# Performance work log

Hardware: AMD Instinct MI355X
Metric: run time of the kernel (lower is better)

The kernel has to match this reference:

```python
import jax, jax.numpy as jnp
import numpy as np

N = 2048
D_T = 256; D_F = 256
E_T = 32; E_F = 32; E_C = 128
C = 5; Q = 512


def setup_inputs() -> dict:
    key = jax.random.key(0)
    ks = jax.random.split(key, 12)
    # full graph minus self-loops, row-major (matches dense_to_sparse ordering)
    r, c = np.meshgrid(np.arange(N), np.arange(N), indexing='ij')
    m = r != c
    edge_index = jnp.asarray(np.stack([r[m], c[m]]), dtype=jnp.int32)  # [2, N*(N-1)]
    E = edge_index.shape[1]
    s = 0.02
    return {
        'time_features': jax.random.normal(ks[0], (N, D_T), jnp.float32),
        'edge_index': edge_index,
        'time_edge_weight': jax.random.uniform(ks[1], (E,), jnp.float32),
        'freq_features': jax.random.normal(ks[2], (N, D_F), jnp.float32),
        'freq_edge_weight': jax.random.uniform(ks[3], (E,), jnp.float32),
        'labels': jax.random.randint(ks[4], (N,), 0, C, jnp.int32),
        'num_classes': C,
        'query_size': Q,
        'Wt': jax.random.normal(ks[5], (D_T, E_T), jnp.float32) * s,
        'bt': jnp.zeros((E_T,), jnp.float32),
        'Wf': jax.random.normal(ks[6], (D_F, E_F), jnp.float32) * s,
        'bf': jnp.zeros((E_F,), jnp.float32),
        'Wc': jax.random.normal(ks[7], (E_T + E_F + C, E_C), jnp.float32) * s,
        'bc': jnp.zeros((E_C,), jnp.float32),
        'Wo': jax.random.normal(ks[8], (E_C, C), jnp.float32) * s,
        'bo': jnp.zeros((C,), jnp.float32),
    }


def _gcn(x, A, W, b):
    # torch_geometric GCNConv: D^{-1/2}(A + I)D^{-1/2} (X W) + b
    n = A.shape[0]
    Ah = A + jnp.eye(n, dtype=A.dtype)
    deg = Ah.sum(axis=1)
    dis = jnp.where(deg > 0, jax.lax.rsqrt(deg), 0.0)
    return (dis[:, None] * Ah * dis[None, :]) @ (x @ W) + b


def reference(time_features, edge_index, time_edge_weight, freq_features,
              freq_edge_weight, labels, num_classes, query_size,
              Wt, bt, Wf, bf, Wc, bc, Wo, bo):
    n = time_features.shape[0]
    lrelu = lambda z: jax.nn.leaky_relu(z, 0.01)

    def dense_adj(w):  # A[dst, src] = w
        return jnp.zeros((n, n), w.dtype).at[edge_index[1], edge_index[0]].add(w)

    te = lrelu(_gcn(time_features, dense_adj(time_edge_weight), Wt, bt))
    fe = lrelu(_gcn(freq_features, dense_adj(freq_edge_weight), Wf, bf))

    # to_one_hot: one_hot[:n - query_size, labels] = 1 -> support rows get 1 in
    # every column that appears anywhere in `labels`
    cols = jnp.zeros((num_classes,), te.dtype).at[labels].set(1.0)
    rowmask = (jnp.arange(n) < (n - query_size)).astype(te.dtype)
    one_hot = rowmask[:, None] * cols[None, :]

    feats = jnp.concatenate([te, fe, one_hot], axis=-1)  # [n, E_T+E_F+C]

    # graph_construction (no_grad in original): 1 / (L1 distance over the
    # non-one-hot dims + 1e-5), zero diagonal
    fd = jax.lax.stop_gradient(feats[:, : feats.shape[1] - num_classes])
    dist = jnp.sum(jnp.abs(fd[:, None, :] - fd[None, :, :]), axis=-1)  # [n, n]
    Aw = (1.0 / (dist + 1e-5)) * (1.0 - jnp.eye(n, dtype=feats.dtype))

    emb = lrelu(_gcn(feats, Aw, Wc, bc))
    return emb @ Wo + bo
```

## Files before the change

### kernel.cpp

```cpp
#include <hip/hip_runtime.h>
#include <hip/hip_bf16.h>

#define N 2048
#define NM1 2047
#define DT 256
#define ET 32
#define EC 128
#define NC 5
#define FS 80
#define FD 69
#define KC_ET 16
#define KC_EC 16

typedef __hip_bfloat16 bf16;

__global__ __launch_bounds__(256) void k_deg_label(const float* __restrict__ tw,
                                                   const float* __restrict__ fw,
                                                   const int* __restrict__ labels,
                                                   float* __restrict__ degT,
                                                   float* __restrict__ degF,
                                                   float* __restrict__ cols){
    int b = blockIdx.x;
    int t = threadIdx.x;
    if (b == 512){
        __shared__ float lc[NC];
        if (t < NC) lc[t] = 0.f;
        __syncthreads();
        for (int i = t; i < N; i += 256){
            int l = labels[i];
            if (l >= 0 && l < NC) lc[l] = 1.f;
        }
        __syncthreads();
        if (t < NC) cols[t] = lc[t];
        return;
    }
    int p = (b & 7)*256 + t;
    if (p >= NM1) return;
    int s0 = (b >> 3)*32;
    float lowT=0.f, highT=0.f, lowF=0.f, highF=0.f;
    #pragma unroll 8
    for (int r = 0; r < 32; ++r){
        int s = s0 + r;
        float vt = tw[(size_t)s*NM1 + p];
        float vf = fw[(size_t)s*NM1 + p];
        if (s <= p){ highT += vt; highF += vf; }
        else       { lowT  += vt; lowF  += vf; }
    }
    atomicAdd(&degT[p],   lowT);
    atomicAdd(&degF[p],   lowF);
    atomicAdd(&degT[p+1], highT);
    atomicAdd(&degF[p+1], highF);
}

__global__ __launch_bounds__(256) void k_xw2(const float* __restrict__ Xt,
                                             const float* __restrict__ Wt,
                                             const float* __restrict__ degT,
                                             float* __restrict__ Zt,
                                             const float* __restrict__ Xf,
                                             const float* __restrict__ Wf,
                                             const float* __restrict__ degF,
                                             float* __restrict__ Zf){
    const float* X   = blockIdx.y ? Xf   : Xt;
    const float* W   = blockIdx.y ? Wf   : Wt;
    const float* deg = blockIdx.y ? degF : degT;
    float*       Z   = blockIdx.y ? Zf   : Zt;
    __shared__ float Ws[DT*ET];
    __shared__ float Xs[8*DT];
    int t = threadIdx.x;
    for (int idx = t; idx < DT*ET; idx += 256) Ws[idx] = W[idx];
    int i0 = blockIdx.x*8;
    for (int idx = t; idx < 8*DT; idx += 256) Xs[idx] = X[(size_t)i0*DT + idx];
    __syncthreads();
    int r = t >> 5, f = t & 31;
    const float* xr = Xs + r*DT;
    float acc = 0.f;
    #pragma unroll 8
    for (int d = 0; d < DT; ++d) acc += xr[d]*Ws[d*ET+f];
    int i = i0 + r;
    Z[(size_t)i*ET+f] = rsqrtf(1.f + deg[i])*acc;
}

__global__ __launch_bounds__(256) void k_agg_et(const float* __restrict__ tw,
                                                const float* __restrict__ fw,
                                                const float* __restrict__ Zt,
                                                const float* __restrict__ Zf,
                                                float* __restrict__ Pt,
                                                float* __restrict__ Pf){
    __shared__ float Ast[64*68];
    __shared__ float Asf[64*68];
    __shared__ float Zst[64*ET];
    __shared__ float Zsf[64*ET];
    int t = threadIdx.x;
    int i0 = blockIdx.x*64;
    int kc = blockIdx.y;
    int k0 = kc*128;
    int g  = t >> 7;
    int tt = t & 127;
    int ig = tt >> 3, fg = tt & 7;
    int r0 = ig*4, c0 = fg*4;
    const float* As = g ? Asf : Ast;
    const float* Zs = g ? Zsf : Zst;
    float acc[4][4];
    #pragma unroll
    for (int u=0;u<4;++u)
        #pragma unroll
        for (int v=0;v<4;++v) acc[u][v]=0.f;

    for (int kt = 0; kt < 2; ++kt){
        int kb = k0 + kt*64;
        #pragma unroll
        for (int e = 0; e < 16; ++e){
            int id = t + e*256;
            int k_l = id >> 6, i_l = id & 63;
            int k = kb + k_l;
            int gi = i0 + i_l;
            float vt, vf;
            if (gi == k){ vt = 0.f; vf = 0.f; }
            else {
                size_t base = (size_t)k*NM1 + gi - (gi > k ? 1 : 0);
                vt = tw[base]; vf = fw[base];
            }
            Ast[k_l*68 + i_l] = vt;
            Asf[k_l*68 + i_l] = vf;
        }
        #pragma unroll
        for (int e = 0; e < 2; ++e){
            int id = t + e*256;
            int row = id >> 3;
            int c4  = (id & 7)*4;
            *(float4*)&Zst[row*ET + c4] = *(const float4*)&Zt[(size_t)(kb+row)*ET + c4];
            *(float4*)&Zsf[row*ET + c4] = *(const float4*)&Zf[(size_t)(kb+row)*ET + c4];
        }
        __syncthreads();
        for (int k = 0; k < 64; ++k){
            float4 a = *(const float4*)&As[k*68 + r0];
            float4 z = *(const float4*)&Zs[k*ET + c0];
            const float* ap = (const float*)&a;
            const float* zp = (const float*)&z;
            #pragma unroll
            for (int u = 0; u < 4; ++u)
                #pragma unroll
                for (int v = 0; v < 4; ++v)
                    acc[u][v] += ap[u]*zp[v];
        }
        __syncthreads();
    }
    float* P = g ? Pf : Pt;
    #pragma unroll
    for (int u = 0; u < 4; ++u){
        size_t ii = (size_t)(i0 + r0 + u);
        float4 o;
        float* po = (float*)&o;
        #pragma unroll
        for (int v = 0; v < 4; ++v) po[v]=acc[u][v];
        *(float4*)&P[(size_t)kc*(N*ET) + ii*ET + c0] = o;
    }
}

__global__ __launch_bounds__(256) void k_feats_epi(const float* __restrict__ Pt,
                                                   const float* __restrict__ Pf,
                                                   const float* __restrict__ Zt,
                                                   const float* __restrict__ Zf,
                                                   const float* __restrict__ degT,
                                                   const float* __restrict__ degF,
                                                   const float* __restrict__ bt,
                                                   const float* __restrict__ bfv,
                                                   const float* __restrict__ cols,
                                                   const int* __restrict__ qsize,
                                                   float* __restrict__ feats){
    int idx = blockIdx.x*256 + threadIdx.x;
    int i = idx >> 6;
    int f = idx & 63;
    float s, rd, b;
    if (f < ET){
        s = Zt[(size_t)i*ET + f];
        #pragma unroll
        for (int kc = 0; kc < KC_ET; ++kc) s += Pt[(size_t)kc*(N*ET) + (size_t)i*ET + f];
        rd = rsqrtf(1.f + degT[i]);
        b = bt[f];
    } else {
        int g = f - ET;
        s = Zf[(size_t)i*ET + g];
        #pragma unroll
        for (int kc = 0; kc < KC_ET; ++kc) s += Pf[(size_t)kc*(N*ET) + (size_t)i*ET + g];
        rd = rsqrtf(1.f + degF[i]);
        b = bfv[g];
    }
    float v = rd*s + b;
    feats[(size_t)i*FS + f] = v > 0.f ? v : 0.01f*v;
    if (f < NC){
        int nsup = N - qsize[0];
        feats[(size_t)i*FS + 2*ET + f] = (i < nsup) ? cols[f] : 0.f;
    }
}

__global__ __launch_bounds__(256) void k_build_aw(const float* __restrict__ feats,
                                                  float* __restrict__ Aw,
                                                  float* __restrict__ dsum){
    __shared__ float fiT[64*68];
    __shared__ float fjT[64*68];
    int t = threadIdx.x;
    int i0 = blockIdx.x*64, j0 = blockIdx.y*64;
    {
        int row = t >> 2;
        int cb  = (t & 3)*16;
        const float4* si = (const float4*)(feats + (size_t)(i0+row)*FS + cb);
        const float4* sj = (const float4*)(feats + (size_t)(j0+row)*FS + cb);
        #pragma unroll
        for (int s = 0; s < 4; ++s){
            float4 v = si[s];
            float4 w = sj[s];
            int c = cb + s*4;
            fiT[(c+0)*68+row]=v.x; fiT[(c+1)*68+row]=v.y; fiT[(c+2)*68+row]=v.z; fiT[(c+3)*68+row]=v.w;
            fjT[(c+0)*68+row]=w.x; fjT[(c+1)*68+row]=w.y; fjT[(c+2)*68+row]=w.z; fjT[(c+3)*68+row]=w.w;
        }
    }
    __syncthreads();
    int tx = t & 15, ty = t >> 4;
    float acc[4][4];
    #pragma unroll
    for (int u=0;u<4;++u)
        #pragma unroll
        for (int v=0;v<4;++v) acc[u][v]=0.f;
    for (int d = 0; d < 64; ++d){
        float4 a4 = *(const float4*)&fiT[d*68 + ty*4];
        float4 b4 = *(const float4*)&fjT[d*68 + tx*4];
        const float* ap = (const float*)&a4;
        const float* bp = (const float*)&b4;
        #pragma unroll
        for (int u = 0; u < 4; ++u)
            #pragma unroll
            for (int v = 0; v < 4; ++v)
                acc[u][v] += fabsf(ap[u]-bp[v]);
    }
    #pragma unroll
    for (int u = 0; u < 4; ++u){
        int gi = i0 + ty*4 + u;
        float4 o;
        float* po = (float*)&o;
        #pragma unroll
        for (int v = 0; v < 4; ++v){
            int gj = j0 + tx*4 + v;
            po[v] = (gi==gj) ? 1.0f : 1.0f/(acc[u][v] + 1e-5f);
        }
        *(float4*)&Aw[(size_t)gi*N + j0 + tx*4] = o;
        float rs = (po[0]+po[1]) + (po[2]+po[3]);
        rs += __shfl_xor(rs, 1);
        rs += __shfl_xor(rs, 2);
        rs += __shfl_xor(rs, 4);
        rs += __shfl_xor(rs, 8);
        if (tx == 0) atomicAdd(&dsum[gi], rs);
    }
}

__global__ __launch_bounds__(256) void k_featswc(const float* __restrict__ feats,
                                                 const float* __restrict__ Wc,
                                                 const float* __restrict__ dsum,
                                                 float* __restrict__ Zc){
    __shared__ float Wcs[FD*EC];
    __shared__ float fr[8][FD+3];
    int t = threadIdx.x;
    for (int idx = t; idx < FD*EC; idx += 256) Wcs[idx] = Wc[idx];
    int i0 = blockIdx.x*8;
    for (int idx = t; idx < 8*FD; idx += 256){
        int r = idx / FD;
        int c = idx - r*FD;
        fr[r][c] = feats[(size_t)(i0+r)*FS + c];
    }
    __syncthreads();
    int f  = t & 127;
    int rh = t >> 7;
    for (int rr = 0; rr < 4; ++rr){
        int r = rh*4 + rr;
        float acc = 0.f;
        #pragma unroll
        for (int d = 0; d < FD; ++d) acc += fr[r][d]*Wcs[d*EC+f];
        int i = i0 + r;
        Zc[(size_t)i*EC + f] = rsqrtf(dsum[i])*acc;
    }
}

__global__ __launch_bounds__(256) void k_agg_ec(const float* __restrict__ Aw,
                                                const float* __restrict__ Zc,
                                                float* __restrict__ Pe){
    __shared__ float As[64*128];
    __shared__ float Zs[64*128];
    int t = threadIdx.x;
    int i0 = blockIdx.x*128;
    int kc = blockIdx.y;
    int k0 = kc*128;
    int rg = t >> 4;
    int cg = t & 15;
    int r0 = rg*8;
    int ca = cg*4, cb = 64 + cg*4;
    float acc[8][8];
    #pragma unroll
    for (int u=0;u<8;++u)
        #pragma unroll
        for (int v=0;v<8;++v) acc[u][v]=0.f;

    for (int kt = 0; kt < 2; ++kt){
        int kb = k0 + kt*64;
        #pragma unroll
        for (int e = 0; e < 8; ++e){
            int id = t + e*256;
            int k_l = id >> 5;
            int i4  = (id & 31)*4;
            *(float4*)&As[k_l*128 + i4] = *(const float4*)&Aw[(size_t)(kb+k_l)*N + i0 + i4];
        }
        #pragma unroll
        for (int e = 0; e < 8; ++e){
            int id = t + e*256;
            int row = id >> 5;
            int c4  = (id & 31)*4;
            *(float4*)&Zs[row*128 + c4] = *(const float4*)&Zc[(size_t)(kb+row)*EC + c4];
        }
        __syncthreads();
        for (int k = 0; k < 64; ++k){
            float4 a0 = *(const float4*)&As[k*128 + r0];
            float4 a1 = *(const float4*)&As[k*128 + r0 + 4];
            float4 z0 = *(const float4*)&Zs[k*128 + ca];
            float4 z1 = *(const float4*)&Zs[k*128 + cb];
            float a8[8] = {a0.x,a0.y,a0.z,a0.w,a1.x,a1.y,a1.z,a1.w};
            float zl[4] = {z0.x,z0.y,z0.z,z0.w};
            float zh[4] = {z1.x,z1.y,z1.z,z1.w};
            #pragma unroll
            for (int u = 0; u < 8; ++u){
                #pragma unroll
                for (int v = 0; v < 4; ++v){
                    acc[u][v]   += a8[u]*zl[v];
                    acc[u][v+4] += a8[u]*zh[v];
                }
            }
        }
        __syncthreads();
    }
    #pragma unroll
    for (int u = 0; u < 8; ++u){
        size_t ii = (size_t)(i0 + r0 + u);
        float4 o0, o1;
        float* p0 = (float*)&o0; float* p1 = (float*)&o1;
        #pragma unroll
        for (int v = 0; v < 4; ++v){ p0[v]=acc[u][v]; p1[v]=acc[u][v+4]; }
        *(float4*)&Pe[(size_t)kc*(N*EC) + ii*EC + ca] = o0;
        *(float4*)&Pe[(size_t)kc*(N*EC) + ii*EC + cb] = o1;
    }
}

__global__ __launch_bounds__(256) void k_embfinal(const float* __restrict__ Pe,
                                                  const float* __restrict__ dsum,
                                                  const float* __restrict__ bc,
                                                  const float* __restrict__ Wo,
                                                  const float* __restrict__ bo,
                                                  float* __restrict__ out){
    __shared__ float vs[2][EC];
    __shared__ float Wos[EC*NC];
    __shared__ float bos[NC];
    int t = threadIdx.x;
    for (int idx = t; idx < EC*NC; idx += 256) Wos[idx] = Wo[idx];
    if (t < NC) bos[t] = bo[t];
    int rr = t >> 7, f = t & 127;
    int i = blockIdx.x*2 + rr;
    size_t idx = (size_t)i*EC + f;
    float s = 0.f;
    #pragma unroll
    for (int kc = 0; kc < KC_EC; ++kc) s += Pe[(size_t)kc*(N*EC) + idx];
    float v = rsqrtf(dsum[i])*s + bc[f];
    vs[rr][f] = v > 0.f ? v : 0.01f*v;
    __syncthreads();
    if (t < 2*NC){
        int r = t / NC;
        int c = t - r*NC;
        float a = bos[c];
        #pragma unroll 8
        for (int f2 = 0; f2 < EC; ++f2) a += vs[r][f2]*Wos[f2*NC+c];
        out[(size_t)(blockIdx.x*2 + r)*NC + c] = a;
    }
}

extern "C" void kernel_launch(void* const* d_in, const int* in_sizes, int n_in,
                              void* d_out, int out_size, void* d_ws, size_t ws_size,
                              hipStream_t stream) {
    const float* time_features = (const float*)d_in[0];
    const float* tw            = (const float*)d_in[2];
    const float* freq_features = (const float*)d_in[3];
    const float* fw            = (const float*)d_in[4];
    const int*   labels        = (const int*)d_in[5];
    const int*   qsize         = (const int*)d_in[7];
    const float* Wt  = (const float*)d_in[8];
    const float* bt  = (const float*)d_in[9];
    const float* Wf  = (const float*)d_in[10];
    const float* bfv = (const float*)d_in[11];
    const float* Wc  = (const float*)d_in[12];
    const float* bc  = (const float*)d_in[13];
    const float* Wo  = (const float*)d_in[14];
    const float* bo  = (const float*)d_in[15];
    float* out = (float*)d_out;

    float* ws    = (float*)d_ws;
    float* Zt    = ws;
    float* Zf    = Zt + (size_t)N*ET;
    float* Zc    = Zf + (size_t)N*ET;
    float* degT  = Zc + (size_t)N*EC;
    float* degF  = degT + N;
    float* dsum  = degF + N;
    float* colsb = dsum + N;
    float* feats = colsb + 8;
    float* Aw    = feats + (size_t)N*FS;
    float* Pt    = Aw + (size_t)N*N;
    float* Pf    = Pt + (size_t)KC_ET*N*ET;
    float* Pe    = Pf + (size_t)KC_ET*N*ET;

    hipMemsetAsync(degT, 0, 3*N*sizeof(float), stream);
    k_deg_label<<<513, 256, 0, stream>>>(tw, fw, labels, degT, degF, colsb);
    k_xw2<<<dim3(N/8, 2), 256, 0, stream>>>(time_features, Wt, degT, Zt,
                                            freq_features, Wf, degF, Zf);
    k_agg_et<<<dim3(N/64, KC_ET), 256, 0, stream>>>(tw, fw, Zt, Zf, Pt, Pf);
    k_feats_epi<<<(N*64)/256, 256, 0, stream>>>(Pt, Pf, Zt, Zf, degT, degF,
                                                bt, bfv, colsb, qsize, feats);
    k_build_aw<<<dim3(N/64, N/64), 256, 0, stream>>>(feats, Aw, dsum);
    k_featswc<<<N/8, 256, 0, stream>>>(feats, Wc, dsum, Zc);
    k_agg_ec<<<dim3(N/128, KC_EC), 256, 0, stream>>>(Aw, Zc, Pe);
    k_embfinal<<<N/2, 256, 0, stream>>>(Pe, dsum, bc, Wo, bo, out);
}
```

Baseline: 212.1 us.

## Exploit Aw symmetry and defer degree scaling out of the XW kernel

The L1-distance adjacency build now computes only upper-triangular 64x64 tiles. It writes each off-diagonal tile twice, once transposed, and adds its column sums into the degree vector, which roughly halves the distance arithmetic. The XW kernel no longer depends on the degree results, so it is launched before the degree kernel, and the rsqrt degree scaling moves into the aggregation load and the epilogue. The cost is a transposed scalar store pattern, strided by N, that is poorly coalesced, plus half the grid exiting immediately.

```diff
diff --git a/kernel.cpp b/kernel.cpp
--- a/kernel.cpp
+++ b/kernel.cpp
@@ -52,18 +52,15 @@
     atomicAdd(&degF[p+1], highF);
 }
 
-__global__ __launch_bounds__(256) void k_xw2(const float* __restrict__ Xt,
-                                             const float* __restrict__ Wt,
-                                             const float* __restrict__ degT,
-                                             float* __restrict__ Zt,
-                                             const float* __restrict__ Xf,
-                                             const float* __restrict__ Wf,
-                                             const float* __restrict__ degF,
-                                             float* __restrict__ Zf){
-    const float* X   = blockIdx.y ? Xf   : Xt;
-    const float* W   = blockIdx.y ? Wf   : Wt;
-    const float* deg = blockIdx.y ? degF : degT;
-    float*       Z   = blockIdx.y ? Zf   : Zt;
+__global__ __launch_bounds__(256) void k_xw(const float* __restrict__ Xt,
+                                            const float* __restrict__ Wt,
+                                            float* __restrict__ Yt,
+                                            const float* __restrict__ Xf,
+                                            const float* __restrict__ Wf,
+                                            float* __restrict__ Yf){
+    const float* X = blockIdx.y ? Xf : Xt;
+    const float* W = blockIdx.y ? Wf : Wt;
+    float*       Y = blockIdx.y ? Yf : Yt;
     __shared__ float Ws[DT*ET];
     __shared__ float Xs[8*DT];
     int t = threadIdx.x;
@@ -76,14 +73,15 @@
     float acc = 0.f;
     #pragma unroll 8
     for (int d = 0; d < DT; ++d) acc += xr[d]*Ws[d*ET+f];
-    int i = i0 + r;
-    Z[(size_t)i*ET+f] = rsqrtf(1.f + deg[i])*acc;
+    Y[(size_t)(i0+r)*ET+f] = acc;
 }
 
 __global__ __launch_bounds__(256) void k_agg_et(const float* __restrict__ tw,
                                                 const float* __restrict__ fw,
-                                                const float* __restrict__ Zt,
-                                                const float* __restrict__ Zf,
+                                                const float* __restrict__ Yt,
+                                                const float* __restrict__ Yf,
+                                                const float* __restrict__ degT,
+                                                const float* __restrict__ degF,
                                                 float* __restrict__ Pt,
                                                 float* __restrict__ Pf){
     __shared__ float Ast[64*68];
@@ -128,8 +126,14 @@
             int id = t + e*256;
             int row = id >> 3;
             int c4  = (id & 7)*4;
-            *(float4*)&Zst[row*ET + c4] = *(const float4*)&Zt[(size_t)(kb+row)*ET + c4];
-            *(float4*)&Zsf[row*ET + c4] = *(const float4*)&Zf[(size_t)(kb+row)*ET + c4];
+            float rdT = rsqrtf(1.f + degT[kb+row]);
+            float rdF = rsqrtf(1.f + degF[kb+row]);
+            float4 yt = *(const float4*)&Yt[(size_t)(kb+row)*ET + c4];
+            float4 yf = *(const float4*)&Yf[(size_t)(kb+row)*ET + c4];
+            yt.x*=rdT; yt.y*=rdT; yt.z*=rdT; yt.w*=rdT;
+            yf.x*=rdF; yf.y*=rdF; yf.z*=rdF; yf.w*=rdF;
+            *(float4*)&Zst[row*ET + c4] = yt;
+            *(float4*)&Zsf[row*ET + c4] = yf;
         }
         __syncthreads();
         for (int k = 0; k < 64; ++k){
@@ -159,8 +163,8 @@
 
 __global__ __launch_bounds__(256) void k_feats_epi(const float* __restrict__ Pt,
                                                    const float* __restrict__ Pf,
-                                                   const float* __restrict__ Zt,
-                                                   const float* __restrict__ Zf,
+                                                   const float* __restrict__ Yt,
+                                                   const float* __restrict__ Yf,
                                                    const float* __restrict__ degT,
                                                    const float* __restrict__ degF,
                                                    const float* __restrict__ bt,
@@ -173,17 +177,17 @@
     int f = idx & 63;
     float s, rd, b;
     if (f < ET){
-        s = Zt[(size_t)i*ET + f];
+        rd = rsqrtf(1.f + degT[i]);
+        s = rd*Yt[(size_t)i*ET + f];
         #pragma unroll
         for (int kc = 0; kc < KC_ET; ++kc) s += Pt[(size_t)kc*(N*ET) + (size_t)i*ET + f];
-        rd = rsqrtf(1.f + degT[i]);
         b = bt[f];
     } else {
         int g = f - ET;
-        s = Zf[(size_t)i*ET + g];
+        rd = rsqrtf(1.f + degF[i]);
+        s = rd*Yf[(size_t)i*ET + g];
         #pragma unroll
         for (int kc = 0; kc < KC_ET; ++kc) s += Pf[(size_t)kc*(N*ET) + (size_t)i*ET + g];
-        rd = rsqrtf(1.f + degF[i]);
         b = bfv[g];
     }
     float v = rd*s + b;
@@ -197,10 +201,12 @@
 __global__ __launch_bounds__(256) void k_build_aw(const float* __restrict__ feats,
                                                   float* __restrict__ Aw,
                                                   float* __restrict__ dsum){
+    int bi = blockIdx.x, bj = blockIdx.y;
+    if (bi > bj) return;
     __shared__ float fiT[64*68];
     __shared__ float fjT[64*68];
     int t = threadIdx.x;
-    int i0 = blockIdx.x*64, j0 = blockIdx.y*64;
+    int i0 = bi*64, j0 = bj*64;
     {
         int row = t >> 2;
         int cb  = (t & 3)*16;
@@ -233,6 +239,8 @@
             for (int v = 0; v < 4; ++v)
                 acc[u][v] += fabsf(ap[u]-bp[v]);
     }
+    bool offdiag = (bi != bj);
+    float cs[4] = {0.f,0.f,0.f,0.f};
     #pragma unroll
     for (int u = 0; u < 4; ++u){
         int gi = i0 + ty*4 + u;
@@ -244,12 +252,32 @@
             po[v] = (gi==gj) ? 1.0f : 1.0f/(acc[u][v] + 1e-5f);
         }
         *(float4*)&Aw[(size_t)gi*N + j0 + tx*4] = o;
+        if (offdiag){
+            #pragma unroll
+            for (int v = 0; v < 4; ++v){
+                int gj = j0 + tx*4 + v;
+                Aw[(size_t)gj*N + gi] = po[v];
+                cs[v] += po[v];
+            }
+        }
         float rs = (po[0]+po[1]) + (po[2]+po[3]);
         rs += __shfl_xor(rs, 1);
         rs += __shfl_xor(rs, 2);
         rs += __shfl_xor(rs, 4);
         rs += __shfl_xor(rs, 8);
         if (tx == 0) atomicAdd(&dsum[gi], rs);
+    }
+    if (offdiag){
+        #pragma unroll
+        for (int v = 0; v < 4; ++v){
+            cs[v] += __shfl_xor(cs[v], 16);
+            cs[v] += __shfl_xor(cs[v], 32);
+        }
+        if ((t & 48) == 0){
+            #pragma unroll
+            for (int v = 0; v < 4; ++v)
+                atomicAdd(&dsum[j0 + tx*4 + v], cs[v]);
+        }
     }
 }
 
@@ -398,9 +426,9 @@
     float* out = (float*)d_out;
 
     float* ws    = (float*)d_ws;
-    float* Zt    = ws;
-    float* Zf    = Zt + (size_t)N*ET;
-    float* Zc    = Zf + (size_t)N*ET;
+    float* Yt    = ws;
+    float* Yf    = Yt + (size_t)N*ET;
+    float* Zc    = Yf + (size_t)N*ET;
     float* degT  = Zc + (size_t)N*EC;
     float* degF  = degT + N;
     float* dsum  = degF + N;
@@ -412,11 +440,11 @@
     float* Pe    = Pf + (size_t)KC_ET*N*ET;
 
     hipMemsetAsync(degT, 0, 3*N*sizeof(float), stream);
+    k_xw<<<dim3(N/8, 2), 256, 0, stream>>>(time_features, Wt, Yt,
+                                           freq_features, Wf, Yf);
     k_deg_label<<<513, 256, 0, stream>>>(tw, fw, labels, degT, degF, colsb);
-    k_xw2<<<dim3(N/8, 2), 256, 0, stream>>>(time_features, Wt, degT, Zt,
-                                            freq_features, Wf, degF, Zf);
-    k_agg_et<<<dim3(N/64, KC_ET), 256, 0, stream>>>(tw, fw, Zt, Zf, Pt, Pf);
-    k_feats_epi<<<(N*64)/256, 256, 0, stream>>>(Pt, Pf, Zt, Zf, degT, degF,
+    k_agg_et<<<dim3(N/64, KC_ET), 256, 0, stream>>>(tw, fw, Yt, Yf, degT, degF, Pt, Pf);
+    k_feats_epi<<<(N*64)/256, 256, 0, stream>>>(Pt, Pf, Yt, Yf, degT, degF,
                                                 bt, bfv, colsb, qsize, feats);
     k_build_aw<<<dim3(N/64, N/64), 256, 0, stream>>>(feats, Aw, dsum);
     k_featswc<<<N/8, 256, 0, stream>>>(feats, Wc, dsum, Zc);
```

Result: slower. 216.5 us (+2.1%).
